# Optimization experiments

Measured on AMD Instinct MI355X. Metric: run time of the kernel, lower is better.

Reference implementation:

```python
import jax, jax.numpy as jnp
import numpy as np

NEG_INF = -jnp.inf


def setup_inputs() -> dict:
    key = jax.random.key(0)
    ks = jax.random.split(key, 20)
    B, N, M = 8, 1024, 128
    F_OP, F_MA, F_E, OUT, HID = 64, 64, 16, 64, 128
    inp = {
        "x": jax.random.normal(ks[0], (B, N, F_OP), dtype=jnp.float32),
        "y": jax.random.normal(ks[1], (B, M, F_MA), dtype=jnp.float32),
        "z": jax.random.normal(ks[2], (B, N, M, F_E), dtype=jnp.float32),
        "op_adj_in": jax.random.randint(ks[3], (B, N, N), 0, 2, dtype=jnp.int32),
        "ma_adj_in": jax.random.randint(ks[4], (B, N, N), 0, 2, dtype=jnp.int32),
        "op_ma_adj": jax.random.randint(ks[5], (B, N, M), 0, 2, dtype=jnp.int32),
        # learned parameters
        "weight_op": jax.random.normal(ks[6], (F_OP, OUT), dtype=jnp.float32) * 0.1,
        "weight_ma": jax.random.normal(ks[7], (F_MA, OUT), dtype=jnp.float32) * 0.1,
        "weight_edge": jax.random.normal(ks[8], (F_E, OUT), dtype=jnp.float32) * 0.1,
        "attention_op": jax.random.normal(ks[9], (1, 2 * OUT), dtype=jnp.float32) * 0.1,
        "attention_ma": jax.random.normal(ks[10], (1, 3 * OUT), dtype=jnp.float32) * 0.1,
        "w1": jax.random.normal(ks[11], (2 * OUT, HID), dtype=jnp.float32) * 0.1,
        "b1": jnp.zeros((HID,), dtype=jnp.float32),
        "w2": jax.random.normal(ks[12], (HID, HID), dtype=jnp.float32) * 0.1,
        "b2": jnp.zeros((HID,), dtype=jnp.float32),
        "wo": jax.random.normal(ks[13], (HID, OUT), dtype=jnp.float32) * 0.1,
        "bo": jnp.zeros((OUT,), dtype=jnp.float32),
    }
    return inp


def reference(x, y, z, op_adj_in, ma_adj_in, op_ma_adj,
              weight_op, weight_ma, weight_edge, attention_op, attention_ma,
              w1, b1, w2, b2, wo, bo):
    OUT = weight_op.shape[1]
    h = jnp.einsum('bni,io->bno', x, weight_op)  # [B,N,OUT]
    # all_combinations[b,i,j] = cat(h[b,j], h[b,i]); dot with attention_op splits:
    a1 = attention_op[0, :OUT]
    a2 = attention_op[0, OUT:]
    e_op = (h @ a2)[:, :, None] + (h @ a1)[:, None, :]  # [B,N,N]
    e_op = jax.nn.leaky_relu(e_op, negative_slope=0.01)

    adj = (jnp.swapaxes(op_adj_in, 1, 2) + op_adj_in
           + jnp.swapaxes(ma_adj_in, 1, 2) + ma_adj_in)  # [B,N,N]
    row_mask = jnp.all(op_ma_adj == 0, axis=-1)  # [B,N] ops with no machine link
    adj = jnp.where(row_mask[:, :, None], 1, adj)
    att = jnp.where(adj > 0, e_op, NEG_INF)
    attention_in_op = jax.nn.softmax(att, axis=2)
    h_prime_op = jnp.einsum('bij,bjo->bio', attention_in_op, h)  # [B,N,OUT]

    h_ma = jnp.einsum('bmi,io->bmo', y, weight_ma)  # [B,M,OUT]
    h_edge = jnp.einsum('bnmi,io->bnmo', z, weight_edge)  # [B,N,M,OUT]
    # cat([h_op_i, h_ma_j, h_edge_ij]) @ attention_ma split into three dots
    am1 = attention_ma[0, :OUT]
    am2 = attention_ma[0, OUT:2 * OUT]
    am3 = attention_ma[0, 2 * OUT:]
    e_ma = (h @ am1)[:, :, None] + (h_ma @ am2)[:, None, :] + h_edge @ am3  # [B,N,M]
    e_ma = jax.nn.leaky_relu(e_ma, negative_slope=0.01)

    adj2 = jnp.where(row_mask[:, :, None], 1, op_ma_adj)
    att2 = jnp.where(adj2 > 0, e_ma, NEG_INF)
    attention_in_ma = jax.nn.softmax(att2, axis=2)  # [B,N,M]
    h_ma_edge = h_ma[:, None, :, :] + h_edge  # [B,N,M,OUT]
    h_prime_ma = jnp.einsum('bnm,bnmo->bno', attention_in_ma, h_ma_edge) + h

    h_prime = jnp.concatenate([h_prime_op, h_prime_ma], axis=-1)  # [B,N,2*OUT]
    embed = jax.nn.elu(h_prime @ w1 + b1)
    embed = jax.nn.elu(embed @ w2 + b2)
    embed = embed @ wo + bo
    embed = jnp.where(row_mask[:, :, None], 0.0, embed)
    return embed
```

## Files before the change

kernel.cpp:

```cpp
#include <hip/hip_runtime.h>
#include <math.h>

#define BB 8
#define NN 1024
#define MM 128
#define FOUT 64
#define HIDN 128

#define OFF_H       0
#define OFF_HMA     524288
#define OFF_HA1     589824
#define OFF_HA2     598016
#define OFF_HAM1    606208
#define OFF_HMAAM2  614400
#define OFF_RMASK   615424
#define OFF_WAM3    623616
#define OFF_HPRIME  623632
#define OFF_UPACK   1672208
#define OFF_OPMB    1934352
#define OFF_WT1HI   1967120
#define OFF_WT1LO   1975312
#define OFF_WT2HI   1983504
#define OFF_WT2LO   1991696
#define OFF_WTOHI   1999888
#define OFF_WTOLO   2003984
#define OFF_HTHI    2008080
#define OFF_HTLO    2270224

typedef __attribute__((ext_vector_type(8))) short bf16x8;
typedef __attribute__((ext_vector_type(8))) unsigned short u16x8;
typedef __attribute__((ext_vector_type(4))) float f32x4;

__device__ __forceinline__ void splitbf(float v, unsigned short& h, unsigned short& l) {
    unsigned u = __float_as_uint(v);
    unsigned hb = (u + 0x7FFFu + ((u >> 16) & 1u)) >> 16;
    float hf = __uint_as_float(hb << 16);
    float lf = v - hf;
    unsigned ul = __float_as_uint(lf);
    unsigned lb = (ul + 0x7FFFu + ((ul >> 16) & 1u)) >> 16;
    h = (unsigned short)hb; l = (unsigned short)lb;
}

__global__ __launch_bounds__(256) void k1_prep(
    const float* __restrict__ x, const float* __restrict__ y,
    const int* __restrict__ op_ma_adj,
    const int* __restrict__ op_adj, const int* __restrict__ ma_adj,
    const float* __restrict__ w_op, const float* __restrict__ w_ma,
    const float* __restrict__ w_edge,
    const float* __restrict__ att_op, const float* __restrict__ att_ma,
    const float* __restrict__ w1_g, const float* __restrict__ w2_g,
    const float* __restrict__ wo_g,
    float* __restrict__ h, float* __restrict__ h_ma,
    float* __restrict__ ha1, float* __restrict__ ha2, float* __restrict__ ham1,
    float* __restrict__ hmaam2, int* __restrict__ rmask, float* __restrict__ wam3,
    unsigned* __restrict__ upack, unsigned long long* __restrict__ opmb,
    unsigned short* __restrict__ wt1hi, unsigned short* __restrict__ wt1lo,
    unsigned short* __restrict__ wt2hi, unsigned short* __restrict__ wt2lo,
    unsigned short* __restrict__ wtohi, unsigned short* __restrict__ wtolo,
    unsigned short* __restrict__ hthi, unsigned short* __restrict__ htlo)
{
    __shared__ float wlds[64 * 64];
    int bid = blockIdx.x;
    int t = threadIdx.x;
    int lane = t & 63;
    int wv = t >> 6;

    if (bid < 2048) {
        for (int k = t; k < 4096; k += 256) wlds[k] = w_op[k];
        __syncthreads();
        int row = bid * 4 + wv;
        float xv = x[(size_t)row * 64 + lane];
        float acc = 0.f;
        #pragma unroll
        for (int i = 0; i < 64; ++i) {
            float xi = __shfl(xv, i);
            acc += xi * wlds[i * 64 + lane];
        }
        h[(size_t)row * 64 + lane] = acc;
        {
            unsigned short hs, ls;
            splitbf(acc, hs, ls);
            size_t tb = ((size_t)((row >> 10) * 64 + lane)) * 1024 + (row & 1023);
            hthi[tb] = hs; htlo[tb] = ls;
        }
        float d1 = acc * att_op[lane];
        float d2 = acc * att_op[64 + lane];
        float d3 = acc * att_ma[lane];
        #pragma unroll
        for (int m = 32; m; m >>= 1) {
            d1 += __shfl_xor(d1, m);
            d2 += __shfl_xor(d2, m);
            d3 += __shfl_xor(d3, m);
        }
        int v0 = op_ma_adj[(size_t)row * 128 + lane];
        int v1 = op_ma_adj[(size_t)row * 128 + 64 + lane];
        unsigned long long w0 = __ballot(v0 != 0);
        unsigned long long w1 = __ballot(v1 != 0);
        if (lane == 0) {
            ha1[row] = d1; ha2[row] = d2; ham1[row] = d3;
            opmb[row * 2] = w0; opmb[row * 2 + 1] = w1;
            rmask[row] = ((w0 | w1) == 0ULL) ? 1 : 0;
        }
    } else if (bid < 2048 + 256) {
        for (int k = t; k < 4096; k += 256) wlds[k] = w_ma[k];
        __syncthreads();
        int row = (bid - 2048) * 4 + wv;
        float yv = y[(size_t)row * 64 + lane];
        float acc = 0.f;
        #pragma unroll
        for (int i = 0; i < 64; ++i) {
            float yi = __shfl(yv, i);
            acc += yi * wlds[i * 64 + lane];
        }
        h_ma[(size_t)row * 64 + lane] = acc;
        float d = acc * att_ma[64 + lane];
        #pragma unroll
        for (int m = 32; m; m >>= 1) d += __shfl_xor(d, m);
        if (lane == 0) hmaam2[row] = d;
    } else if (bid == 2304) {
        if (t < 16) {
            float s = 0.f;
            for (int o = 0; o < 64; ++o) s += w_edge[t * 64 + o] * att_ma[128 + o];
            wam3[t] = s;
        }
    } else if (bid < 3393) {
        unsigned* sAB = (unsigned*)wlds;
        int p = bid - 2305;
        int b = p / 136;
        int pr = p % 136;
        int I = 0;
        { int rem = pr, cnt = 16;
          while (rem >= cnt) { rem -= cnt; cnt--; I++; }
          pr = rem; }
        int J = I + pr;

        int c = t & 63, hr = (t >> 6) & 1, ts = t >> 7;
        int Ia = ts ? J : I, Ja = ts ? I : J;
        const int* opb = op_adj + (size_t)b * NN * NN + (size_t)(Ia * 64) * NN + Ja * 64;
        const int* mab = ma_adj + (size_t)b * NN * NN + (size_t)(Ia * 64) * NN + Ja * 64;
        unsigned w = 0;
        #pragma unroll 8
        for (int k = 0; k < 32; ++k) {
            int r = hr * 32 + k;
            int aval = opb[(size_t)r * NN + c] | mab[(size_t)r * NN + c];
            w |= (aval ? 1u : 0u) << k;
        }
        sAB[ts * 128 + c * 2 + hr] = w;
        __syncthreads();
        if (t < 128) {
            int r = t & 63, hh = t >> 6;
            int rw = r >> 5, rb = r & 31;
            unsigned dir1 = sAB[128 + r * 2 + hh];
            unsigned dir2 = sAB[r * 2 + hh];
            unsigned wt1 = 0, wt2 = 0;
            #pragma unroll 8
            for (int k = 0; k < 32; ++k) {
                int cc = hh * 32 + k;
                wt1 |= ((sAB[cc * 2 + rw] >> rb) & 1u) << k;
                wt2 |= ((sAB[128 + cc * 2 + rw] >> rb) & 1u) << k;
            }
            upack[((size_t)(b * NN + I * 64 + r)) * 32 + J * 2 + hh] = dir1 | wt1;
            upack[((size_t)(b * NN + J * 64 + r)) * 32 + I * 2 + hh] = dir2 | wt2;
        }
    } else {
        float (*tls)[33] = (float(*)[33])wlds;
        int p = bid - 3393;
        const float* src; unsigned short *dhi, *dlo; int KD, CD, tI, tJ;
        if (p < 16)      { src = w1_g; dhi = wt1hi; dlo = wt1lo; KD = 128; CD = 128; tI = p >> 2; tJ = p & 3; }
        else if (p < 32) { src = w2_g; dhi = wt2hi; dlo = wt2lo; KD = 128; CD = 128; tI = (p-16) >> 2; tJ = (p-16) & 3; }
        else             { src = wo_g; dhi = wtohi; dlo = wtolo; KD = 128; CD = 64;  tI = (p-32) >> 1; tJ = (p-32) & 1; }
        int k0 = tI * 32, c0 = tJ * 32;
        #pragma unroll
        for (int it = 0; it < 4; ++it) {
            int r = (t >> 5) + it * 8;
            int c = t & 31;
            tls[r][c] = src[(size_t)(k0 + r) * CD + c0 + c];
        }
        __syncthreads();
        #pragma unroll
        for (int it = 0; it < 4; ++it) {
            int c = (t >> 5) + it * 8;
            int k = t & 31;
            unsigned short hs, ls;
            splitbf(tls[k][c], hs, ls);
            dhi[(size_t)(c0 + c) * KD + k0 + k] = hs;
            dlo[(size_t)(c0 + c) * KD + k0 + k] = ls;
        }
    }
}

__global__ __launch_bounds__(256) void k2_opatt(
    const unsigned* __restrict__ upack,
    const unsigned short* __restrict__ hthi,
    const unsigned short* __restrict__ htlo,
    const float* __restrict__ ha1, const float* __restrict__ ha2,
    const int* __restrict__ rmask, float* __restrict__ h_prime)
{
    __shared__ __align__(16) unsigned short Pl[16 * 1024];
    __shared__ float ha1s[1024];
    __shared__ unsigned uws[512];
    __shared__ float rdeninv[16];
    int bid = blockIdx.x;
    int b = bid >> 6;
    int i0 = (bid & 63) << 4;
    int t = threadIdx.x;

    {
        size_t ub = (size_t)(b * NN + i0) * 32;
        uws[t] = upack[ub + t];
        uws[t + 256] = upack[ub + t + 256];
    }
    ha1s[t] = ha1[b * NN + t];
    ha1s[t + 256] = ha1[b * NN + t + 256];
    ha1s[t + 512] = ha1[b * NN + t + 512];
    ha1s[t + 768] = ha1[b * NN + t + 768];
    __syncthreads();

    {
        int row = t >> 4, q = t & 15;
        int bn = b * NN + i0 + row;
        float ha2i = ha2[bn];
        unsigned rm = rmask[bn] ? 0xFFFFFFFFu : 0u;

        float mx = -INFINITY;
        #pragma unroll 8
        for (int jj = 0; jj < 64; ++jj) {
            int j = q + (jj << 4);
            float ev = ha2i + ha1s[j];
            ev = ev > 0.f ? ev : 0.01f * ev;
            unsigned w = uws[row * 32 + (j >> 5)] | rm;
            if ((w >> (j & 31)) & 1u) mx = fmaxf(mx, ev);
        }
        #pragma unroll
        for (int m = 1; m < 16; m <<= 1) mx = fmaxf(mx, __shfl_xor(mx, m));

        float s = 0.f;
        #pragma unroll 4
        for (int jj = 0; jj < 64; ++jj) {
            int j = q + (jj << 4);
            float ev = ha2i + ha1s[j];
            ev = ev > 0.f ? ev : 0.01f * ev;
            unsigned w = uws[row * 32 + (j >> 5)] | rm;
            float u = ((w >> (j & 31)) & 1u) ? __expf(ev - mx) : 0.f;
            s += u;
            unsigned ub = __float_as_uint(u);
            unsigned short pb = (unsigned short)((ub + 0x7FFFu + ((ub >> 16) & 1u)) >> 16);
            unsigned byteoff = ((unsigned)(row * 2048 + j * 2)) ^ ((unsigned)((row & 7) << 4));
            *(unsigned short*)((char*)Pl + byteoff) = pb;
        }
        #pragma unroll
        for (int m = 1; m < 16; m <<= 1) s += __shfl_xor(s, m);
        if (q == 0) rdeninv[row] = 1.f / s;
    }
    __syncthreads();

    {
        int lane = t & 63, wvv = t >> 6;
        int arow = lane & 15, kg = lane >> 4;
        int col = wvv * 16 + arow;
        const unsigned short* bhp = hthi + ((size_t)(b * 64 + col)) * 1024;
        const unsigned short* blp = htlo + ((size_t)(b * 64 + col)) * 1024;
        f32x4 acc = {0.f, 0.f, 0.f, 0.f};
        #pragma unroll 8
        for (int kst = 0; kst < 32; ++kst) {
            unsigned cc = ((unsigned)(kst * 4 + kg)) ^ ((unsigned)(arow & 7));
            bf16x8 pa = *(const bf16x8*)((char*)Pl + arow * 2048 + cc * 16);
            bf16x8 vh = *(const bf16x8*)&bhp[kst * 32 + kg * 8];
            bf16x8 vl = *(const bf16x8*)&blp[kst * 32 + kg * 8];
            acc = __builtin_amdgcn_mfma_f32_16x16x32_bf16(pa, vh, acc, 0, 0, 0);
            acc = __builtin_amdgcn_mfma_f32_16x16x32_bf16(pa, vl, acc, 0, 0, 0);
        }
        size_t base = (size_t)(b * NN + i0);
        #pragma unroll
        for (int r = 0; r < 4; ++r) {
            int orow = kg * 4 + r;
            float v = acc[r] * rdeninv[orow];
            h_prime[(base + orow) * 128 + col] = v;
        }
    }
}

__global__ __launch_bounds__(256) void k3_maatt(
    const float* __restrict__ z, const unsigned long long* __restrict__ opmb,
    const float* __restrict__ h, const float* __restrict__ h_ma,
    const float* __restrict__ ham1, const float* __restrict__ hmaam2,
    const int* __restrict__ rmask, const float* __restrict__ wam3,
    const float* __restrict__ w_edge, float* __restrict__ h_prime)
{
    __shared__ float hma_s[128 * 64];
    __shared__ float u_s[2][128];
    __shared__ float redmx[4], redsm[4];
    __shared__ float part[2][8][16];
    __shared__ float zsum_s[2][16];
    __shared__ float hmp[2][2][64];
    __shared__ float wam3s[16];
    __shared__ float rdens[2];

    int bid = blockIdx.x;
    int b = bid >> 7;
    int n0 = (bid & 127) * 8;
    int t = threadIdx.x;
    int wvid = t >> 6;

    {
        const float4* src = (const float4*)(h_ma + (size_t)b * MM * 64);
        float4* dst = (float4*)hma_s;
        #pragma unroll
        for (int it = 0; it < 8; ++it) dst[t + 256 * it] = src[t + 256 * it];
    }
    if (t < 16) wam3s[t] = wam3[t];
    __syncthreads();

    for (int pp = 0; pp < 4; ++pp) {
        int nsel = t >> 7;
        int m = t & 127;
        int n = n0 + pp * 2 + nsel;
        int bn = b * NN + n;

        size_t zbase = ((size_t)bn * MM + m) * 16;
        float4 z0 = *(const float4*)(z + zbase);
        float4 z1 = *(const float4*)(z + zbase + 4);
        float4 z2 = *(const float4*)(z + zbase + 8);
        float4 z3 = *(const float4*)(z + zbase + 12);
        float e = ham1[bn] + hmaam2[b * MM + m];
        e += z0.x*wam3s[0] + z0.y*wam3s[1] + z0.z*wam3s[2] + z0.w*wam3s[3];
        e += z1.x*wam3s[4] + z1.y*wam3s[5] + z1.z*wam3s[6] + z1.w*wam3s[7];
        e += z2.x*wam3s[8] + z2.y*wam3s[9] + z2.z*wam3s[10] + z2.w*wam3s[11];
        e += z3.x*wam3s[12] + z3.y*wam3s[13] + z3.z*wam3s[14] + z3.w*wam3s[15];
        e = e > 0.f ? e : 0.01f * e;
        unsigned long long bits = opmb[(size_t)bn * 2 + (m >> 6)];
        int valid = rmask[bn] | (int)((bits >> (m & 63)) & 1ULL);
        e = valid ? e : -INFINITY;

        float mx = e;
        #pragma unroll
        for (int msk = 32; msk; msk >>= 1) mx = fmaxf(mx, __shfl_xor(mx, msk));
        if ((t & 63) == 0) redmx[wvid] = mx;
        __syncthreads();
        mx = fmaxf(redmx[nsel * 2], redmx[nsel * 2 + 1]);
        float uu = __expf(e - mx);
        u_s[nsel][m] = uu;
        float sv = uu;
        #pragma unroll
        for (int msk = 32; msk; msk >>= 1) sv += __shfl_xor(sv, msk);
        if ((t & 63) == 0) redsm[wvid] = sv;
        __syncthreads();
        float den = redsm[nsel * 2] + redsm[nsel * 2 + 1];
        if (m == 0) rdens[nsel] = 1.f / den;

        {
            int i = t & 15;
            int g = (t >> 4) & 7;
            int ns2 = t >> 7;
            int bn2 = b * NN + n0 + pp * 2 + ns2;
            const float* zr = z + (size_t)bn2 * MM * 16;
            float facc = 0.f;
            #pragma unroll
            for (int k = 0; k < 16; ++k) {
                int mm = g * 16 + k;
                facc += u_s[ns2][mm] * zr[(size_t)mm * 16 + i];
            }
            part[ns2][g][i] = facc;
        }
        {
            int o = t & 63;
            int q = (t >> 6) & 1;
            int ns3 = t >> 7;
            float acc = 0.f;
            #pragma unroll 8
            for (int k = 0; k < 64; ++k) {
                int mm = q * 64 + k;
                acc += u_s[ns3][mm] * hma_s[mm * 64 + o];
            }
            hmp[ns3][q][o] = acc;
        }
        __syncthreads();
        if (t < 32) {
            int ns = t >> 4, i = t & 15;
            float zs = 0.f;
            #pragma unroll
            for (int g = 0; g < 8; ++g) zs += part[ns][g][i];
            zsum_s[ns][i] = zs;
        }
        __syncthreads();
        if (t < 128) {
            int ns = t >> 6, oo = t & 63;
            int bnf = b * NN + n0 + pp * 2 + ns;
            float he = 0.f;
            #pragma unroll
            for (int i = 0; i < 16; ++i) he += zsum_s[ns][i] * w_edge[i * 64 + oo];
            float val = (hmp[ns][0][oo] + hmp[ns][1][oo] + he) * rdens[ns]
                      + h[(size_t)bnf * 64 + oo];
            h_prime[(size_t)bnf * 128 + 64 + oo] = val;
        }
        __syncthreads();
    }
}

__global__ __launch_bounds__(256) void k4_mlp(
    const float* __restrict__ hp, const int* __restrict__ rmask,
    const unsigned short* __restrict__ wt1hi, const unsigned short* __restrict__ wt1lo,
    const unsigned short* __restrict__ wt2hi, const unsigned short* __restrict__ wt2lo,
    const unsigned short* __restrict__ wtohi, const unsigned short* __restrict__ wtolo,
    const float* __restrict__ b1, const float* __restrict__ b2,
    const float* __restrict__ bo, float* __restrict__ out)
{
    __shared__ __align__(16) unsigned short Ahi0[16 * 136];
    __shared__ __align__(16) unsigned short Alo0[16 * 136];
    __shared__ __align__(16) unsigned short Ahi1[16 * 136];
    __shared__ __align__(16) unsigned short Alo1[16 * 136];
    __shared__ int rml[16];
    int t = threadIdx.x;
    int lane = t & 63;
    int wv = t >> 6;
    int row0 = blockIdx.x * 16;

    {
        int r = t >> 4;
        int cg = (t & 15) * 8;
        const float* src = hp + (size_t)(row0 + r) * 128 + cg;
        float4 v0 = *(const float4*)src;
        float4 v1 = *(const float4*)(src + 4);
        float xs[8] = {v0.x, v0.y, v0.z, v0.w, v1.x, v1.y, v1.z, v1.w};
        u16x8 hv, lv;
        #pragma unroll
        for (int j = 0; j < 8; ++j) {
            unsigned short hs, ls;
            splitbf(xs[j], hs, ls);
            hv[j] = hs; lv[j] = ls;
        }
        *(u16x8*)&Ahi0[r * 136 + cg] = hv;
        *(u16x8*)&Alo0[r * 136 + cg] = lv;
        if (t < 16) rml[t] = rmask[row0 + t];
    }
    __syncthreads();

    int arow = lane & 15;
    int kg = lane >> 4;
    int aoff = arow * 136 + kg * 8;

    {
        bf16x8 ah[4], al[4];
        #pragma unroll
        for (int ks = 0; ks < 4; ++ks) {
            ah[ks] = *(const bf16x8*)&Ahi0[aoff + ks * 32];
            al[ks] = *(const bf16x8*)&Alo0[aoff + ks * 32];
        }
        #pragma unroll
        for (int q = 0; q < 2; ++q) {
            int ct = wv + q * 4;
            int col = ct * 16 + arow;
            const unsigned short* wh = wt1hi + (size_t)col * 128 + kg * 8;
            const unsigned short* wl = wt1lo + (size_t)col * 128 + kg * 8;
            f32x4 acc = {0.f, 0.f, 0.f, 0.f};
            #pragma unroll
            for (int ks = 0; ks < 4; ++ks) {
                bf16x8 bh = *(const bf16x8*)&wh[ks * 32];
                bf16x8 bl = *(const bf16x8*)&wl[ks * 32];
                acc = __builtin_amdgcn_mfma_f32_16x16x32_bf16(ah[ks], bh, acc, 0, 0, 0);
                acc = __builtin_amdgcn_mfma_f32_16x16x32_bf16(al[ks], bh, acc, 0, 0, 0);
                acc = __builtin_amdgcn_mfma_f32_16x16x32_bf16(ah[ks], bl, acc, 0, 0, 0);
            }
            float bb = b1[col];
            #pragma unroll
            for (int r = 0; r < 4; ++r) {
                int row = kg * 4 + r;
                float v = acc[r] + bb;
                v = v > 0.f ? v : __expf(v) - 1.f;
                unsigned short hs, ls;
                splitbf(v, hs, ls);
                Ahi1[row * 136 + col] = hs;
                Alo1[row * 136 + col] = ls;
            }
        }
    }
    __syncthreads();

    {
        bf16x8 ah[4], al[4];
        #pragma unroll
        for (int ks = 0; ks < 4; ++ks) {
            ah[ks] = *(const bf16x8*)&Ahi1[aoff + ks * 32];
            al[ks] = *(const bf16x8*)&Alo1[aoff + ks * 32];
        }
        #pragma unroll
        for (int q = 0; q < 2; ++q) {
            int ct = wv + q * 4;
            int col = ct * 16 + arow;
            const unsigned short* wh = wt2hi + (size_t)col * 128 + kg * 8;
            const unsigned short* wl = wt2lo + (size_t)col * 128 + kg * 8;
            f32x4 acc = {0.f, 0.f, 0.f, 0.f};
            #pragma unroll
            for (int ks = 0; ks < 4; ++ks) {
                bf16x8 bh = *(const bf16x8*)&wh[ks * 32];
                bf16x8 bl = *(const bf16x8*)&wl[ks * 32];
                acc = __builtin_amdgcn_mfma_f32_16x16x32_bf16(ah[ks], bh, acc, 0, 0, 0);
                acc = __builtin_amdgcn_mfma_f32_16x16x32_bf16(al[ks], bh, acc, 0, 0, 0);
                acc = __builtin_amdgcn_mfma_f32_16x16x32_bf16(ah[ks], bl, acc, 0, 0, 0);
            }
            float bb = b2[col];
            #pragma unroll
            for (int r = 0; r < 4; ++r) {
                int row = kg * 4 + r;
                float v = acc[r] + bb;
                v = v > 0.f ? v : __expf(v) - 1.f;
                unsigned short hs, ls;
                splitbf(v, hs, ls);
                Ahi0[row * 136 + col] = hs;
                Alo0[row * 136 + col] = ls;
            }
        }
    }
    __syncthreads();

    {
        bf16x8 ah[4], al[4];
        #pragma unroll
        for (int ks = 0; ks < 4; ++ks) {
            ah[ks] = *(const bf16x8*)&Ahi0[aoff + ks * 32];
            al[ks] = *(const bf16x8*)&Alo0[aoff + ks * 32];
        }
        int ct = wv;
        int col = ct * 16 + arow;
        const unsigned short* wh = wtohi + (size_t)col * 128 + kg * 8;
        const unsigned short* wl = wtolo + (size_t)col * 128 + kg * 8;
        f32x4 acc = {0.f, 0.f, 0.f, 0.f};
        #pragma unroll
        for (int ks = 0; ks < 4; ++ks) {
            bf16x8 bh = *(const bf16x8*)&wh[ks * 32];
            bf16x8 bl = *(const bf16x8*)&wl[ks * 32];
            acc = __builtin_amdgcn_mfma_f32_16x16x32_bf16(ah[ks], bh, acc, 0, 0, 0);
            acc = __builtin_amdgcn_mfma_f32_16x16x32_bf16(al[ks], bh, acc, 0, 0, 0);
            acc = __builtin_amdgcn_mfma_f32_16x16x32_bf16(ah[ks], bl, acc, 0, 0, 0);
        }
        float bb = bo[col];
        #pragma unroll
        for (int r = 0; r < 4; ++r) {
            int row = kg * 4 + r;
            float v = acc[r] + bb;
            out[(size_t)(row0 + row) * 64 + col] = rml[row] ? 0.f : v;
        }
    }
}

extern "C" void kernel_launch(void* const* d_in, const int* in_sizes, int n_in,
                              void* d_out, int out_size, void* d_ws, size_t ws_size,
                              hipStream_t stream) {
    const float* x      = (const float*)d_in[0];
    const float* y      = (const float*)d_in[1];
    const float* z      = (const float*)d_in[2];
    const int*   op_adj = (const int*)d_in[3];
    const int*   ma_adj = (const int*)d_in[4];
    const int*   opma   = (const int*)d_in[5];
    const float* w_op   = (const float*)d_in[6];
    const float* w_ma   = (const float*)d_in[7];
    const float* w_edge = (const float*)d_in[8];
    const float* att_op = (const float*)d_in[9];
    const float* att_ma = (const float*)d_in[10];
    const float* w1     = (const float*)d_in[11];
    const float* b1     = (const float*)d_in[12];
    const float* w2     = (const float*)d_in[13];
    const float* b2     = (const float*)d_in[14];
    const float* wo     = (const float*)d_in[15];
    const float* bo     = (const float*)d_in[16];
    float* out = (float*)d_out;

    float* ws = (float*)d_ws;
    float* h       = ws + OFF_H;
    float* h_ma    = ws + OFF_HMA;
    float* ha1     = ws + OFF_HA1;
    float* ha2     = ws + OFF_HA2;
    float* ham1    = ws + OFF_HAM1;
    float* hmaam2  = ws + OFF_HMAAM2;
    int*   rmask   = (int*)(ws + OFF_RMASK);
    float* wam3    = ws + OFF_WAM3;
    float* h_prime = ws + OFF_HPRIME;
    unsigned* upack = (unsigned*)(ws + OFF_UPACK);
    unsigned long long* opmb = (unsigned long long*)(ws + OFF_OPMB);
    unsigned short* wt1hi = (unsigned short*)(ws + OFF_WT1HI);
    unsigned short* wt1lo = (unsigned short*)(ws + OFF_WT1LO);
    unsigned short* wt2hi = (unsigned short*)(ws + OFF_WT2HI);
    unsigned short* wt2lo = (unsigned short*)(ws + OFF_WT2LO);
    unsigned short* wtohi = (unsigned short*)(ws + OFF_WTOHI);
    unsigned short* wtolo = (unsigned short*)(ws + OFF_WTOLO);
    unsigned short* hthi  = (unsigned short*)(ws + OFF_HTHI);
    unsigned short* htlo  = (unsigned short*)(ws + OFF_HTLO);

    k1_prep<<<2048 + 256 + 1 + 1088 + 40, 256, 0, stream>>>(
        x, y, opma, op_adj, ma_adj, w_op, w_ma, w_edge, att_op, att_ma,
        w1, w2, wo,
        h, h_ma, ha1, ha2, ham1, hmaam2, rmask, wam3, upack, opmb,
        wt1hi, wt1lo, wt2hi, wt2lo, wtohi, wtolo, hthi, htlo);

    k2_opatt<<<512, 256, 0, stream>>>(
        upack, hthi, htlo, ha1, ha2, rmask, h_prime);

    k3_maatt<<<1024, 256, 0, stream>>>(
        z, opmb, h, h_ma, ham1, hmaam2, rmask, wam3, w_edge, h_prime);

    k4_mlp<<<512, 256, 0, stream>>>(
        h_prime, rmask, wt1hi, wt1lo, wt2hi, wt2lo, wtohi, wtolo,
        b1, b2, bo, out);
}
```

Before: 87.44 us.

## Use MFMA for machine attention aggregation, batch prep rows, ballot-based adjacency packing

Three stages change. The machine-attention kernel now does its weighted sum over h_ma with bf16 MFMA, using hi/lo split bf16 copies of h_ma prepared in the prep kernel, and reduces z with a register shuffle butterfly instead of shared-memory passes. The prep kernel processes 32 rows per block and writes the transposed bf16 copies with vectorised stores. Adjacency bit packing now uses wave ballots and a shuffle-based 64x64 bit transpose. This cuts block counts, LDS traffic and barriers, but the attention weights are rounded to a single bf16 in the MFMA, which lowers precision.

New measurement: 99.43 us. 1.14x slower.

```diff
diff --git a/kernel.cpp b/kernel.cpp
--- a/kernel.cpp
+++ b/kernel.cpp
@@ -26,6 +26,8 @@
 #define OFF_WTOLO   2003984
 #define OFF_HTHI    2008080
 #define OFF_HTLO    2270224
+#define OFF_HMATHI  2532368
+#define OFF_HMATLO  2565136
 
 typedef __attribute__((ext_vector_type(8))) short bf16x8;
 typedef __attribute__((ext_vector_type(8))) unsigned short u16x8;
@@ -57,75 +59,125 @@
     unsigned short* __restrict__ wt1hi, unsigned short* __restrict__ wt1lo,
     unsigned short* __restrict__ wt2hi, unsigned short* __restrict__ wt2lo,
     unsigned short* __restrict__ wtohi, unsigned short* __restrict__ wtolo,
-    unsigned short* __restrict__ hthi, unsigned short* __restrict__ htlo)
+    unsigned short* __restrict__ hthi, unsigned short* __restrict__ htlo,
+    unsigned short* __restrict__ hmathi, unsigned short* __restrict__ hmatlo)
 {
     __shared__ float wlds[64 * 64];
+    __shared__ unsigned hstage[32 * 64];
     int bid = blockIdx.x;
     int t = threadIdx.x;
     int lane = t & 63;
     int wv = t >> 6;
 
-    if (bid < 2048) {
+    if (bid < 256) {
+        int b = bid >> 5;
+        int n0g = (bid & 31) * 32;
         for (int k = t; k < 4096; k += 256) wlds[k] = w_op[k];
-        __syncthreads();
-        int row = bid * 4 + wv;
-        float xv = x[(size_t)row * 64 + lane];
-        float acc = 0.f;
-        #pragma unroll
-        for (int i = 0; i < 64; ++i) {
-            float xi = __shfl(xv, i);
-            acc += xi * wlds[i * 64 + lane];
-        }
-        h[(size_t)row * 64 + lane] = acc;
-        {
+        float a1c = att_op[lane], a2c = att_op[64 + lane], am1c = att_ma[lane];
+        __syncthreads();
+        #pragma unroll
+        for (int p = 0; p < 8; ++p) {
+            int row = b * NN + n0g + p * 4 + wv;
+            float xv = x[(size_t)row * 64 + lane];
+            float acc = 0.f;
+            #pragma unroll
+            for (int i = 0; i < 64; ++i) {
+                float xi = __shfl(xv, i);
+                acc += xi * wlds[i * 64 + lane];
+            }
+            h[(size_t)row * 64 + lane] = acc;
             unsigned short hs, ls;
             splitbf(acc, hs, ls);
-            size_t tb = ((size_t)((row >> 10) * 64 + lane)) * 1024 + (row & 1023);
-            hthi[tb] = hs; htlo[tb] = ls;
-        }
-        float d1 = acc * att_op[lane];
-        float d2 = acc * att_op[64 + lane];
-        float d3 = acc * att_ma[lane];
-        #pragma unroll
-        for (int m = 32; m; m >>= 1) {
-            d1 += __shfl_xor(d1, m);
-            d2 += __shfl_xor(d2, m);
-            d3 += __shfl_xor(d3, m);
-        }
-        int v0 = op_ma_adj[(size_t)row * 128 + lane];
-        int v1 = op_ma_adj[(size_t)row * 128 + 64 + lane];
-        unsigned long long w0 = __ballot(v0 != 0);
-        unsigned long long w1 = __ballot(v1 != 0);
-        if (lane == 0) {
-            ha1[row] = d1; ha2[row] = d2; ham1[row] = d3;
-            opmb[row * 2] = w0; opmb[row * 2 + 1] = w1;
-            rmask[row] = ((w0 | w1) == 0ULL) ? 1 : 0;
-        }
-    } else if (bid < 2048 + 256) {
+            hstage[(p * 4 + wv) * 64 + lane] = (unsigned)hs | ((unsigned)ls << 16);
+            float d1 = acc * a1c, d2 = acc * a2c, d3 = acc * am1c;
+            #pragma unroll
+            for (int m = 32; m; m >>= 1) {
+                d1 += __shfl_xor(d1, m);
+                d2 += __shfl_xor(d2, m);
+                d3 += __shfl_xor(d3, m);
+            }
+            int v0 = op_ma_adj[(size_t)row * 128 + lane];
+            int v1 = op_ma_adj[(size_t)row * 128 + 64 + lane];
+            unsigned long long w0 = __ballot(v0 != 0);
+            unsigned long long w1 = __ballot(v1 != 0);
+            if (lane == 0) {
+                ha1[row] = d1; ha2[row] = d2; ham1[row] = d3;
+                opmb[row * 2] = w0; opmb[row * 2 + 1] = w1;
+                rmask[row] = ((w0 | w1) == 0ULL) ? 1 : 0;
+            }
+        }
+        __syncthreads();
+        {
+            int plane = t >> 7;
+            int q = t & 127;
+            int o = q >> 1;
+            int hf = q & 1;
+            int sh = plane * 16;
+            unsigned short* dst = plane ? htlo : hthi;
+            u16x8 pk0, pk1;
+            #pragma unroll
+            for (int k = 0; k < 8; ++k)
+                pk0[k] = (unsigned short)((hstage[(hf * 16 + k) * 64 + o] >> sh) & 0xFFFFu);
+            #pragma unroll
+            for (int k = 0; k < 8; ++k)
+                pk1[k] = (unsigned short)((hstage[(hf * 16 + 8 + k) * 64 + o] >> sh) & 0xFFFFu);
+            size_t base = ((size_t)(b * 64 + o)) * 1024 + n0g + hf * 16;
+            *(u16x8*)&dst[base] = pk0;
+            *(u16x8*)&dst[base + 8] = pk1;
+        }
+    } else if (bid < 288) {
+        int bb = (bid - 256) >> 2;
+        int m0 = ((bid - 256) & 3) * 32;
         for (int k = t; k < 4096; k += 256) wlds[k] = w_ma[k];
-        __syncthreads();
-        int row = (bid - 2048) * 4 + wv;
-        float yv = y[(size_t)row * 64 + lane];
-        float acc = 0.f;
-        #pragma unroll
-        for (int i = 0; i < 64; ++i) {
-            float yi = __shfl(yv, i);
-            acc += yi * wlds[i * 64 + lane];
-        }
-        h_ma[(size_t)row * 64 + lane] = acc;
-        float d = acc * att_ma[64 + lane];
-        #pragma unroll
-        for (int m = 32; m; m >>= 1) d += __shfl_xor(d, m);
-        if (lane == 0) hmaam2[row] = d;
-    } else if (bid == 2304) {
+        float am2c = att_ma[64 + lane];
+        __syncthreads();
+        #pragma unroll
+        for (int p = 0; p < 8; ++p) {
+            int row = bb * MM + m0 + p * 4 + wv;
+            float yv = y[(size_t)row * 64 + lane];
+            float acc = 0.f;
+            #pragma unroll
+            for (int i = 0; i < 64; ++i) {
+                float yi = __shfl(yv, i);
+                acc += yi * wlds[i * 64 + lane];
+            }
+            h_ma[(size_t)row * 64 + lane] = acc;
+            unsigned short hs, ls;
+            splitbf(acc, hs, ls);
+            hstage[(p * 4 + wv) * 64 + lane] = (unsigned)hs | ((unsigned)ls << 16);
+            float d = acc * am2c;
+            #pragma unroll
+            for (int m = 32; m; m >>= 1) d += __shfl_xor(d, m);
+            if (lane == 0) hmaam2[row] = d;
+        }
+        __syncthreads();
+        {
+            int plane = t >> 7;
+            int q = t & 127;
+            int o = q >> 1;
+            int hf = q & 1;
+            int sh = plane * 16;
+            unsigned short* dst = plane ? hmatlo : hmathi;
+            u16x8 pk0, pk1;
+            #pragma unroll
+            for (int k = 0; k < 8; ++k)
+                pk0[k] = (unsigned short)((hstage[(hf * 16 + k) * 64 + o] >> sh) & 0xFFFFu);
+            #pragma unroll
+            for (int k = 0; k < 8; ++k)
+                pk1[k] = (unsigned short)((hstage[(hf * 16 + 8 + k) * 64 + o] >> sh) & 0xFFFFu);
+            size_t base = ((size_t)(bb * 64 + o)) * 128 + m0 + hf * 16;
+            *(u16x8*)&dst[base] = pk0;
+            *(u16x8*)&dst[base + 8] = pk1;
+        }
+    } else if (bid == 288) {
         if (t < 16) {
             float s = 0.f;
             for (int o = 0; o < 64; ++o) s += w_edge[t * 64 + o] * att_ma[128 + o];
             wam3[t] = s;
         }
-    } else if (bid < 3393) {
-        unsigned* sAB = (unsigned*)wlds;
-        int p = bid - 2305;
+    } else if (bid < 1377) {
+        unsigned long long* rowmask = (unsigned long long*)wlds;
+        int p = bid - 289;
         int b = p / 136;
         int pr = p % 136;
         int I = 0;
@@ -134,37 +186,40 @@
           pr = rem; }
         int J = I + pr;
 
-        int c = t & 63, hr = (t >> 6) & 1, ts = t >> 7;
-        int Ia = ts ? J : I, Ja = ts ? I : J;
-        const int* opb = op_adj + (size_t)b * NN * NN + (size_t)(Ia * 64) * NN + Ja * 64;
-        const int* mab = ma_adj + (size_t)b * NN * NN + (size_t)(Ia * 64) * NN + Ja * 64;
-        unsigned w = 0;
+        int orient = wv >> 1, rhalf = wv & 1;
+        int Ia = orient ? J : I, Ja = orient ? I : J;
+        const int* opb = op_adj + (size_t)b * NN * NN + (size_t)(Ia * 64 + rhalf * 32) * NN + Ja * 64;
+        const int* mab = ma_adj + (size_t)b * NN * NN + (size_t)(Ia * 64 + rhalf * 32) * NN + Ja * 64;
         #pragma unroll 8
-        for (int k = 0; k < 32; ++k) {
-            int r = hr * 32 + k;
-            int aval = opb[(size_t)r * NN + c] | mab[(size_t)r * NN + c];
-            w |= (aval ? 1u : 0u) << k;
-        }
-        sAB[ts * 128 + c * 2 + hr] = w;
-        __syncthreads();
-        if (t < 128) {
-            int r = t & 63, hh = t >> 6;
-            int rw = r >> 5, rb = r & 31;
-            unsigned dir1 = sAB[128 + r * 2 + hh];
-            unsigned dir2 = sAB[r * 2 + hh];
-            unsigned wt1 = 0, wt2 = 0;
-            #pragma unroll 8
-            for (int k = 0; k < 32; ++k) {
-                int cc = hh * 32 + k;
-                wt1 |= ((sAB[cc * 2 + rw] >> rb) & 1u) << k;
-                wt2 |= ((sAB[128 + cc * 2 + rw] >> rb) & 1u) << k;
-            }
-            upack[((size_t)(b * NN + I * 64 + r)) * 32 + J * 2 + hh] = dir1 | wt1;
-            upack[((size_t)(b * NN + J * 64 + r)) * 32 + I * 2 + hh] = dir2 | wt2;
+        for (int rr = 0; rr < 32; ++rr) {
+            int v = opb[(size_t)rr * NN + lane] | mab[(size_t)rr * NN + lane];
+            unsigned long long bm = __ballot(v != 0);
+            if (lane == 0) rowmask[orient * 64 + rhalf * 32 + rr] = bm;
+        }
+        __syncthreads();
+        if (wv < 2) {
+            unsigned long long xx = rowmask[(wv ^ 1) * 64 + lane];
+            const unsigned long long M1  = 0x5555555555555555ULL;
+            const unsigned long long M2  = 0x3333333333333333ULL;
+            const unsigned long long M4  = 0x0F0F0F0F0F0F0F0FULL;
+            const unsigned long long M8  = 0x00FF00FF00FF00FFULL;
+            const unsigned long long M16 = 0x0000FFFF0000FFFFULL;
+            const unsigned long long M32 = 0x00000000FFFFFFFFULL;
+            unsigned long long yv_;
+            yv_ = __shfl_xor(xx, 1);  xx = (lane & 1)  ? ((xx & ~M1)  | ((yv_ >> 1)  & M1))  : ((xx & M1)  | ((yv_ << 1)  & ~M1));
+            yv_ = __shfl_xor(xx, 2);  xx = (lane & 2)  ? ((xx & ~M2)  | ((yv_ >> 2)  & M2))  : ((xx & M2)  | ((yv_ << 2)  & ~M2));
+            yv_ = __shfl_xor(xx, 4);  xx = (lane & 4)  ? ((xx & ~M4)  | ((yv_ >> 4)  & M4))  : ((xx & M4)  | ((yv_ << 4)  & ~M4));
+            yv_ = __shfl_xor(xx, 8);  xx = (lane & 8)  ? ((xx & ~M8)  | ((yv_ >> 8)  & M8))  : ((xx & M8)  | ((yv_ << 8)  & ~M8));
+            yv_ = __shfl_xor(xx, 16); xx = (lane & 16) ? ((xx & ~M16) | ((yv_ >> 16) & M16)) : ((xx & M16) | ((yv_ << 16) & ~M16));
+            yv_ = __shfl_xor(xx, 32); xx = (lane & 32) ? ((xx & ~M32) | ((yv_ >> 32) & M32)) : ((xx & M32) | ((yv_ << 32) & ~M32));
+            unsigned long long res = rowmask[wv * 64 + lane] | xx;
+            int R = wv ? J : I, C = wv ? I : J;
+            size_t idx = ((size_t)(b * NN + R * 64 + lane)) * 32 + C * 2;
+            *(unsigned long long*)&upack[idx] = res;
         }
     } else {
         float (*tls)[33] = (float(*)[33])wlds;
-        int p = bid - 3393;
+        int p = bid - 1377;
         const float* src; unsigned short *dhi, *dlo; int KD, CD, tI, tJ;
         if (p < 16)      { src = w1_g; dhi = wt1hi; dlo = wt1lo; KD = 128; CD = 128; tI = p >> 2; tJ = p & 3; }
         else if (p < 32) { src = w2_g; dhi = wt2hi; dlo = wt2lo; KD = 128; CD = 128; tI = (p-16) >> 2; tJ = (p-16) & 3; }
@@ -282,51 +337,55 @@
 
 __global__ __launch_bounds__(256) void k3_maatt(
     const float* __restrict__ z, const unsigned long long* __restrict__ opmb,
-    const float* __restrict__ h, const float* __restrict__ h_ma,
+    const float* __restrict__ h,
+    const unsigned short* __restrict__ hmathi, const unsigned short* __restrict__ hmatlo,
     const float* __restrict__ ham1, const float* __restrict__ hmaam2,
     const int* __restrict__ rmask, const float* __restrict__ wam3,
     const float* __restrict__ w_edge, float* __restrict__ h_prime)
 {
-    __shared__ float hma_s[128 * 64];
-    __shared__ float u_s[2][128];
+    __shared__ __align__(16) unsigned short U_lds[16 * 136];
+    __shared__ float wedge_s[1024];
+    __shared__ float wam3s[16];
+    __shared__ float zsum_s[16][16];
+    __shared__ float zpart[4][16];
     __shared__ float redmx[4], redsm[4];
-    __shared__ float part[2][8][16];
-    __shared__ float zsum_s[2][16];
-    __shared__ float hmp[2][2][64];
-    __shared__ float wam3s[16];
-    __shared__ float rdens[2];
+    __shared__ float rdeninv[16];
 
     int bid = blockIdx.x;
-    int b = bid >> 7;
-    int n0 = (bid & 127) * 8;
+    int b = bid >> 6;
+    int n0 = (bid & 63) * 16;
     int t = threadIdx.x;
+    int lane = t & 63;
     int wvid = t >> 6;
-
-    {
-        const float4* src = (const float4*)(h_ma + (size_t)b * MM * 64);
-        float4* dst = (float4*)hma_s;
-        #pragma unroll
-        for (int it = 0; it < 8; ++it) dst[t + 256 * it] = src[t + 256 * it];
-    }
+    int ns = t >> 7;
+    int m = t & 127;
+
+    for (int k = t; k < 1024; k += 256) wedge_s[k] = w_edge[k];
     if (t < 16) wam3s[t] = wam3[t];
     __syncthreads();
 
-    for (int pp = 0; pp < 4; ++pp) {
-        int nsel = t >> 7;
-        int m = t & 127;
-        int n = n0 + pp * 2 + nsel;
+    float hmam2v = hmaam2[b * MM + m];
+
+    for (int pp = 0; pp < 8; ++pp) {
+        int n = n0 + pp * 2 + ns;
         int bn = b * NN + n;
 
-        size_t zbase = ((size_t)bn * MM + m) * 16;
-        float4 z0 = *(const float4*)(z + zbase);
-        float4 z1 = *(const float4*)(z + zbase + 4);
-        float4 z2 = *(const float4*)(z + zbase + 8);
-        float4 z3 = *(const float4*)(z + zbase + 12);
-        float e = ham1[bn] + hmaam2[b * MM + m];
-        e += z0.x*wam3s[0] + z0.y*wam3s[1] + z0.z*wam3s[2] + z0.w*wam3s[3];
-        e += z1.x*wam3s[4] + z1.y*wam3s[5] + z1.z*wam3s[6] + z1.w*wam3s[7];
-        e += z2.x*wam3s[8] + z2.y*wam3s[9] + z2.z*wam3s[10] + z2.w*wam3s[11];
-        e += z3.x*wam3s[12] + z3.y*wam3s[13] + z3.z*wam3s[14] + z3.w*wam3s[15];
+        float zv[16];
+        {
+            size_t zbase = ((size_t)bn * MM + m) * 16;
+            float4 z0 = *(const float4*)(z + zbase);
+            float4 z1 = *(const float4*)(z + zbase + 4);
+            float4 z2 = *(const float4*)(z + zbase + 8);
+            float4 z3 = *(const float4*)(z + zbase + 12);
+            zv[0]=z0.x; zv[1]=z0.y; zv[2]=z0.z; zv[3]=z0.w;
+            zv[4]=z1.x; zv[5]=z1.y; zv[6]=z1.z; zv[7]=z1.w;
+            zv[8]=z2.x; zv[9]=z2.y; zv[10]=z2.z; zv[11]=z2.w;
+            zv[12]=z3.x; zv[13]=z3.y; zv[14]=z3.z; zv[15]=z3.w;
+        }
+
+        float e = ham1[bn] + hmam2v;
+        #pragma unroll
+        for (int i = 0; i < 16; ++i) e += zv[i] * wam3s[i];
         e = e > 0.f ? e : 0.01f * e;
         unsigned long long bits = opmb[(size_t)bn * 2 + (m >> 6)];
         int valid = rmask[bn] | (int)((bits >> (m & 63)) & 1ULL);
@@ -335,65 +394,89 @@
         float mx = e;
         #pragma unroll
         for (int msk = 32; msk; msk >>= 1) mx = fmaxf(mx, __shfl_xor(mx, msk));
-        if ((t & 63) == 0) redmx[wvid] = mx;
-        __syncthreads();
-        mx = fmaxf(redmx[nsel * 2], redmx[nsel * 2 + 1]);
+        if (lane == 0) redmx[wvid] = mx;
+        __syncthreads();
+        mx = fmaxf(redmx[ns * 2], redmx[ns * 2 + 1]);
         float uu = __expf(e - mx);
-        u_s[nsel][m] = uu;
+
+        {
+            unsigned ub = __float_as_uint(uu);
+            unsigned short pb = (unsigned short)((ub + 0x7FFFu + ((ub >> 16) & 1u)) >> 16);
+            U_lds[(pp * 2 + ns) * 136 + m] = pb;
+        }
+
         float sv = uu;
         #pragma unroll
         for (int msk = 32; msk; msk >>= 1) sv += __shfl_xor(sv, msk);
-        if ((t & 63) == 0) redsm[wvid] = sv;
-        __syncthreads();
-        float den = redsm[nsel * 2] + redsm[nsel * 2 + 1];
-        if (m == 0) rdens[nsel] = 1.f / den;
-
+        if (lane == 0) redsm[wvid] = sv;
+
+        #pragma unroll
+        for (int i = 0; i < 16; ++i) zv[i] *= uu;
+        #pragma unroll
+        for (int s2 = 0; s2 < 8; ++s2) {
+            float sel = (lane & 1) ? zv[s2] : zv[s2 + 8];
+            float got = __shfl_xor(sel, 1);
+            zv[s2] = ((lane & 1) ? zv[s2 + 8] : zv[s2]) + got;
+        }
+        #pragma unroll
+        for (int s2 = 0; s2 < 4; ++s2) {
+            float sel = (lane & 2) ? zv[s2] : zv[s2 + 4];
+            float got = __shfl_xor(sel, 2);
+            zv[s2] = ((lane & 2) ? zv[s2 + 4] : zv[s2]) + got;
+        }
+        #pragma unroll
+        for (int s2 = 0; s2 < 2; ++s2) {
+            float sel = (lane & 4) ? zv[s2] : zv[s2 + 2];
+            float got = __shfl_xor(sel, 4);
+            zv[s2] = ((lane & 4) ? zv[s2 + 2] : zv[s2]) + got;
+        }
         {
-            int i = t & 15;
-            int g = (t >> 4) & 7;
-            int ns2 = t >> 7;
-            int bn2 = b * NN + n0 + pp * 2 + ns2;
-            const float* zr = z + (size_t)bn2 * MM * 16;
-            float facc = 0.f;
-            #pragma unroll
-            for (int k = 0; k < 16; ++k) {
-                int mm = g * 16 + k;
-                facc += u_s[ns2][mm] * zr[(size_t)mm * 16 + i];
-            }
-            part[ns2][g][i] = facc;
-        }
-        {
-            int o = t & 63;
-            int q = (t >> 6) & 1;
-            int ns3 = t >> 7;
-            float acc = 0.f;
-            #pragma unroll 8
-            for (int k = 0; k < 64; ++k) {
-                int mm = q * 64 + k;
-                acc += u_s[ns3][mm] * hma_s[mm * 64 + o];
-            }
-            hmp[ns3][q][o] = acc;
+            float sel = (lane & 8) ? zv[0] : zv[1];
+            float got = __shfl_xor(sel, 8);
+            zv[0] = ((lane & 8) ? zv[1] : zv[0]) + got;
+        }
+        zv[0] += __shfl_xor(zv[0], 16);
+        zv[0] += __shfl_xor(zv[0], 32);
+        if (lane < 16) {
+            int comp = ((lane & 1) << 3) | ((lane & 2) << 1) | ((lane & 4) >> 1) | ((lane & 8) >> 3);
+            zpart[wvid][comp] = zv[0];
         }
         __syncthreads();
         if (t < 32) {
-            int ns = t >> 4, i = t & 15;
-            float zs = 0.f;
-            #pragma unroll
-            for (int g = 0; g < 8; ++g) zs += part[ns][g][i];
-            zsum_s[ns][i] = zs;
-        }
-        __syncthreads();
-        if (t < 128) {
-            int ns = t >> 6, oo = t & 63;
-            int bnf = b * NN + n0 + pp * 2 + ns;
+            int ns2 = t >> 4, i = t & 15;
+            zsum_s[pp * 2 + ns2][i] = zpart[ns2 * 2][i] + zpart[ns2 * 2 + 1][i];
+        }
+        if ((t & 127) == 0) rdeninv[pp * 2 + ns] = 1.f / (redsm[ns * 2] + redsm[ns * 2 + 1]);
+        __syncthreads();
+    }
+
+    {
+        int arow = lane & 15, kg = lane >> 4;
+        int col = wvid * 16 + arow;
+        bf16x8 ua[4];
+        #pragma unroll
+        for (int ks = 0; ks < 4; ++ks)
+            ua[ks] = *(const bf16x8*)&U_lds[arow * 136 + kg * 8 + ks * 32];
+        const unsigned short* bhp = hmathi + ((size_t)(b * 64 + col)) * 128 + kg * 8;
+        const unsigned short* blp = hmatlo + ((size_t)(b * 64 + col)) * 128 + kg * 8;
+        f32x4 acc = {0.f, 0.f, 0.f, 0.f};
+        #pragma unroll
+        for (int ks = 0; ks < 4; ++ks) {
+            bf16x8 bh = *(const bf16x8*)&bhp[ks * 32];
+            bf16x8 bl = *(const bf16x8*)&blp[ks * 32];
+            acc = __builtin_amdgcn_mfma_f32_16x16x32_bf16(ua[ks], bh, acc, 0, 0, 0);
+            acc = __builtin_amdgcn_mfma_f32_16x16x32_bf16(ua[ks], bl, acc, 0, 0, 0);
+        }
+        #pragma unroll
+        for (int r = 0; r < 4; ++r) {
+            int row = kg * 4 + r;
             float he = 0.f;
             #pragma unroll
-            for (int i = 0; i < 16; ++i) he += zsum_s[ns][i] * w_edge[i * 64 + oo];
-            float val = (hmp[ns][0][oo] + hmp[ns][1][oo] + he) * rdens[ns]
-                      + h[(size_t)bnf * 64 + oo];
-            h_prime[(size_t)bnf * 128 + 64 + oo] = val;
-        }
-        __syncthreads();
+            for (int i = 0; i < 16; ++i) he += zsum_s[row][i] * wedge_s[i * 64 + col];
+            int bn = b * NN + n0 + row;
+            float val = (acc[r] + he) * rdeninv[row] + h[(size_t)bn * 64 + col];
+            h_prime[(size_t)bn * 128 + 64 + col] = val;
+        }
     }
 }
 
@@ -585,18 +668,20 @@
     unsigned short* wtolo = (unsigned short*)(ws + OFF_WTOLO);
     unsigned short* hthi  = (unsigned short*)(ws + OFF_HTHI);
     unsigned short* htlo  = (unsigned short*)(ws + OFF_HTLO);
-
-    k1_prep<<<2048 + 256 + 1 + 1088 + 40, 256, 0, stream>>>(
+    unsigned short* hmathi = (unsigned short*)(ws + OFF_HMATHI);
+    unsigned short* hmatlo = (unsigned short*)(ws + OFF_HMATLO);
+
+    k1_prep<<<256 + 32 + 1 + 1088 + 40, 256, 0, stream>>>(
         x, y, opma, op_adj, ma_adj, w_op, w_ma, w_edge, att_op, att_ma,
         w1, w2, wo,
         h, h_ma, ha1, ha2, ham1, hmaam2, rmask, wam3, upack, opmb,
-        wt1hi, wt1lo, wt2hi, wt2lo, wtohi, wtolo, hthi, htlo);
+        wt1hi, wt1lo, wt2hi, wt2lo, wtohi, wtolo, hthi, htlo, hmathi, hmatlo);
 
     k2_opatt<<<512, 256, 0, stream>>>(
         upack, hthi, htlo, ha1, ha2, rmask, h_prime);
 
-    k3_maatt<<<1024, 256, 0, stream>>>(
-        z, opmb, h, h_ma, ham1, hmaam2, rmask, wam3, w_edge, h_prime);
+    k3_maatt<<<512, 256, 0, stream>>>(
+        z, opmb, h, hmathi, hmatlo, ham1, hmaam2, rmask, wam3, w_edge, h_prime);
 
     k4_mlp<<<512, 256, 0, stream>>>(
         h_prime, rmask, wt1hi, wt1lo, wt2hi, wt2lo, wtohi, wtolo,
```
